# Performance work log

Hardware: AMD Instinct MI355X
Metric: run time of the kernel (lower is better)

Reference implementation:

```python
import jax, jax.numpy as jnp
import numpy as np

NW, NS, E = 50000, 10000, 100000
H, C = 6, 300            # heads, out_channels (word_size)
DIN_S, DIN_W = 640, 300  # sentence_size, word_size
DHID = 2048              # FFN hidden


def setup_inputs() -> dict:
    key = jax.random.key(0)
    ks = jax.random.split(key, 12)
    Hw = jax.random.normal(ks[0], (NW, DIN_W), dtype=jnp.float32)
    Hs = jax.random.normal(ks[1], (NS, DIN_S), dtype=jnp.float32)
    src = jax.random.randint(ks[2], (E,), 0, NS)
    dst = jax.random.randint(ks[3], (E,), 0, NW)
    s2w = jnp.stack([src, dst]).astype(jnp.int64)  # [2, E] edge_index
    # GATConv params (bipartite): lin_src, lin_dst, att_src, att_dst, bias
    Wsrc = jax.random.normal(ks[4], (H * C, DIN_S), dtype=jnp.float32) / np.sqrt(DIN_S)
    Wdst = jax.random.normal(ks[5], (H * C, DIN_W), dtype=jnp.float32) / np.sqrt(DIN_W)
    att_src = jax.random.normal(ks[6], (H, C), dtype=jnp.float32) / np.sqrt(C)
    att_dst = jax.random.normal(ks[7], (H, C), dtype=jnp.float32) / np.sqrt(C)
    bias_gat = jnp.zeros((H * C,), dtype=jnp.float32)
    # FFN params: Linear(1800 -> 2048), Linear(2048 -> 300)
    W1 = jax.random.normal(ks[8], (DHID, H * C), dtype=jnp.float32) / np.sqrt(H * C)
    b1 = jnp.zeros((DHID,), dtype=jnp.float32)
    W2 = jax.random.normal(ks[9], (DIN_W, DHID), dtype=jnp.float32) / np.sqrt(DHID)
    b2 = jnp.zeros((DIN_W,), dtype=jnp.float32)
    return dict(Hw=Hw, Hs=Hs, s2w=s2w, Wsrc=Wsrc, Wdst=Wdst, att_src=att_src,
                att_dst=att_dst, bias_gat=bias_gat, W1=W1, b1=b1, W2=W2, b2=b2)


def reference(Hw, Hs, s2w, Wsrc, Wdst, att_src, att_dst, bias_gat, W1, b1, W2, b2):
    nw = Hw.shape[0]
    src, dst = s2w[0], s2w[1]
    h, c = att_src.shape
    # edge-wise linear transforms (done node-wise, then gathered)
    xs = (Hs @ Wsrc.T).reshape(-1, h, c)   # [Ns, H, C]
    xd = (Hw @ Wdst.T).reshape(-1, h, c)   # [Nw, H, C]
    a_s = jnp.einsum('nhc,hc->nh', xs, att_src)  # [Ns, H]
    a_d = jnp.einsum('nhc,hc->nh', xd, att_dst)  # [Nw, H]
    alpha = a_s[src] + a_d[dst]                  # [E, H]
    alpha = jnp.where(alpha > 0, alpha, 0.2 * alpha)  # leaky_relu(0.2)
    # segment softmax over edges grouped by destination word
    m = jax.ops.segment_max(alpha, dst, num_segments=nw)      # [Nw, H]
    ex = jnp.exp(alpha - m[dst])                               # [E, H]
    den = jax.ops.segment_sum(ex, dst, num_segments=nw)       # [Nw, H]
    w = ex / den[dst]                                          # [E, H]
    msg = xs[src] * w[:, :, None]                              # [E, H, C]
    agg = jax.ops.segment_sum(msg, dst, num_segments=nw)      # [Nw, H, C]
    Uw = agg.reshape(nw, h * c) + bias_gat                     # concat heads + bias
    # activation (elu), dropout treated as identity (deterministic reference)
    Uw = jax.nn.elu(Uw)
    # FFN with residual to Hw
    out = (Uw @ W1.T + b1) @ W2.T + b2 + Hw
    return out
```

## Files before the change

### kernel.cpp

```cpp
#include <hip/hip_runtime.h>
#include <hip/hip_bf16.h>
#include <math.h>

#define NWn 50000
#define NSn 10000
#define NEn 100000
#define Hn  6
#define DWn 300
#define DSn 640
#define DHn 2048
#define HCn 1800
#define HCp 1824
#define K32 57
#define NFB 19
#define CHUNK 10000
#define ENC_NEGINF 0x007FFFFFu

typedef short bf16x8 __attribute__((ext_vector_type(8)));
typedef float f32x4  __attribute__((ext_vector_type(4)));

__device__ __forceinline__ unsigned enc_ord(float f) {
  unsigned u = __float_as_uint(f);
  return (u & 0x80000000u) ? ~u : (u | 0x80000000u);
}
__device__ __forceinline__ float dec_ord(unsigned u) {
  unsigned v = (u & 0x80000000u) ? (u ^ 0x80000000u) : ~u;
  return __uint_as_float(v);
}
__device__ __forceinline__ float eluf(float x) { return x > 0.0f ? x : expm1f(x); }
__device__ __forceinline__ float b2f(short s) {
  return __uint_as_float(((unsigned)(unsigned short)s) << 16);
}
__device__ __forceinline__ short f2b(float f) {
  __hip_bfloat16 h = __float2bfloat16(f);
  return *(short*)&h;
}

__device__ __forceinline__ int ld_src(const int* s32, int e, int f) {
  return f ? s32[2 * e] : s32[e];
}
__device__ __forceinline__ int ld_dst(const int* s32, int e, int f) {
  return f ? s32[2 * NEn + 2 * e] : s32[NEn + e];
}

__global__ __launch_bounds__(256) void k_init(unsigned* m_enc, float* den, int* deg,
                                              int* cur, int* flag, float* Vs, float* Vd) {
  int i = blockIdx.x * 256 + threadIdx.x;
  if (i < NWn * Hn) { m_enc[i] = ENC_NEGINF; den[i] = 0.0f; }
  if (i < NWn) { deg[i] = 0; cur[i] = 0; }
  if (i < Hn * DSn) Vs[i] = 0.f;
  if (i < Hn * DWn) Vd[i] = 0.f;
  if (i == 0) *flag = 1;
}

__global__ __launch_bounds__(256) void k_detect(const int* __restrict__ s32, int* flag) {
  int j = threadIdx.x;
  if (s32[2 * j + 1] != 0) atomicAnd(flag, 0);
}

__global__ __launch_bounds__(256) void k_cvt(const float* __restrict__ src,
    __hip_bfloat16* __restrict__ dst, int n4) {
  int i = blockIdx.x * 256 + threadIdx.x;
  if (i >= n4) return;
  float4 v = *(const float4*)&src[(size_t)i * 4];
  __hip_bfloat16 o[4] = {__float2bfloat16(v.x), __float2bfloat16(v.y),
                         __float2bfloat16(v.z), __float2bfloat16(v.w)};
  *(ulong1*)&dst[(size_t)i * 4] = *(ulong1*)o;
}

__global__ __launch_bounds__(256) void k_tcvt(const float* __restrict__ W1,
    __hip_bfloat16* __restrict__ W1t) {
  __shared__ __hip_bfloat16 T[64][65];
  int tid = threadIdx.x;
  int tx = tid & 15, ty = tid >> 4;
  int c0 = blockIdx.x * 64;
  int r0 = blockIdx.y * 64;
  #pragma unroll
  for (int rr = 0; rr < 4; ++rr) {
    int sr = r0 + rr * 16 + ty;
    int sc = c0 + tx * 4;
    float4 v;
    if (sc + 3 < HCn) {
      v = *(const float4*)&W1[(size_t)sr * HCn + sc];
    } else {
      v.x = (sc + 0 < HCn) ? W1[(size_t)sr * HCn + sc + 0] : 0.f;
      v.y = (sc + 1 < HCn) ? W1[(size_t)sr * HCn + sc + 1] : 0.f;
      v.z = (sc + 2 < HCn) ? W1[(size_t)sr * HCn + sc + 2] : 0.f;
      v.w = (sc + 3 < HCn) ? W1[(size_t)sr * HCn + sc + 3] : 0.f;
    }
    T[tx * 4 + 0][rr * 16 + ty] = __float2bfloat16(v.x);
    T[tx * 4 + 1][rr * 16 + ty] = __float2bfloat16(v.y);
    T[tx * 4 + 2][rr * 16 + ty] = __float2bfloat16(v.z);
    T[tx * 4 + 3][rr * 16 + ty] = __float2bfloat16(v.w);
  }
  __syncthreads();
  #pragma unroll
  for (int ww = 0; ww < 4; ++ww) {
    int dl = ww * 16 + ty;
    int dr = c0 + dl;
    if (dr >= HCn) continue;
    __hip_bfloat16 o[4] = {T[dl][tx * 4 + 0], T[dl][tx * 4 + 1],
                           T[dl][tx * 4 + 2], T[dl][tx * 4 + 3]};
    *(uint2*)&W1t[(size_t)dr * DHn + r0 + tx * 4] = *(uint2*)o;
  }
}

#define VCC 6
__global__ __launch_bounds__(256) void k_vsd(const float* __restrict__ Wsrc,
    const float* __restrict__ Wdst, const float* __restrict__ att_src,
    const float* __restrict__ att_dst, float* __restrict__ Vs, float* __restrict__ Vd) {
  int b = blockIdx.x;
  bool isD = b >= Hn * VCC;
  int bb = isD ? b - Hn * VCC : b;
  int h = bb / VCC, cc = bb % VCC;
  int cbeg = h * 300 + cc * 50, cend = cbeg + 50;
  if (!isD) {
    for (int k = threadIdx.x; k < DSn; k += 256) {
      float s = 0.f;
      for (int c = cbeg; c < cend; ++c)
        s = fmaf(att_src[c], Wsrc[(size_t)c * DSn + k], s);
      unsafeAtomicAdd(&Vs[h * DSn + k], s);
    }
  } else {
    for (int k = threadIdx.x; k < DWn; k += 256) {
      float s = 0.f;
      for (int c = cbeg; c < cend; ++c)
        s = fmaf(att_dst[c], Wdst[(size_t)c * DWn + k], s);
      unsafeAtomicAdd(&Vd[h * DWn + k], s);
    }
  }
}

__global__ __launch_bounds__(256) void k_rowdot(const float* __restrict__ X,
    const float* __restrict__ V, float* __restrict__ outv, int nrows, int K) {
  extern __shared__ float VL[];
  for (int i = threadIdx.x; i < Hn * K; i += 256) VL[i] = V[i];
  __syncthreads();
  int row = blockIdx.x * 4 + (threadIdx.x >> 6);
  int lane = threadIdx.x & 63;
  if (row >= nrows) return;
  float acc[Hn] = {0.f, 0.f, 0.f, 0.f, 0.f, 0.f};
  const float* xr = X + (size_t)row * K;
  for (int k = lane; k < K; k += 64) {
    float x = xr[k];
    #pragma unroll
    for (int h = 0; h < Hn; ++h) acc[h] = fmaf(x, VL[h * K + k], acc[h]);
  }
  #pragma unroll
  for (int h = 0; h < Hn; ++h) {
    float v = acc[h];
    for (int ofs = 32; ofs > 0; ofs >>= 1) v += __shfl_down(v, ofs);
    if (lane == 0) outv[(size_t)row * Hn + h] = v;
  }
}

__global__ __launch_bounds__(256) void k_bc(const float* __restrict__ W2,
    const float* __restrict__ b1, const float* __restrict__ b2, float* __restrict__ bc) {
  int j = blockIdx.x * 4 + (threadIdx.x >> 6);
  int lane = threadIdx.x & 63;
  if (j >= DWn) return;
  float s = 0.f;
  for (int t = lane; t < DHn; t += 64) s = fmaf(W2[(size_t)j * DHn + t], b1[t], s);
  for (int ofs = 32; ofs > 0; ofs >>= 1) s += __shfl_down(s, ofs);
  if (lane == 0) bc[j] = s + b2[j];
}

template <int EPI>
__global__ __launch_bounds__(256) void k_mfma(
    const __hip_bfloat16* __restrict__ A, const __hip_bfloat16* __restrict__ B,
    void* __restrict__ Cout, int M, int N, int K, int lda, int ldb, int ldc) {
  __shared__ short As[2][128 * 32];
  __shared__ short Bs[2][128 * 32];
  int tid = threadIdx.x, lane = tid & 63, wid = tid >> 6;
  int wr = wid >> 1, wc = wid & 1;
  int m0 = blockIdx.y * 128, n0 = blockIdx.x * 128;
  int z = blockIdx.z;
  int ksp = K / (int)gridDim.z;
  int kbeg = z * ksp;
  int nt = ksp / 32;
  auto STAGE = [&](int buf, int kk) {
    #pragma unroll
    for (int i = 0; i < 2; ++i) {
      int slotbase = wid * 128 + i * 64;
      int s = slotbase + lane;
      int row = s >> 2, kq = (s & 3) ^ ((row >> 1) & 3);
      int gm = m0 + row; if (gm > M - 1) gm = M - 1;
      const __hip_bfloat16* gsa = A + (size_t)gm * lda + kk + kq * 8;
      __builtin_amdgcn_global_load_lds(
          (const __attribute__((address_space(1))) void*)gsa,
          (__attribute__((address_space(3))) void*)&As[buf][slotbase * 8], 16, 0, 0);
      int gn = n0 + row; if (gn > N - 1) gn = N - 1;
      const __hip_bfloat16* gsb = B + (size_t)gn * ldb + kk + kq * 8;
      __builtin_amdgcn_global_load_lds(
          (const __attribute__((address_space(1))) void*)gsb,
          (__attribute__((address_space(3))) void*)&Bs[buf][slotbase * 8], 16, 0, 0);
    }
  };
  f32x4 acc[4][4] = {};
  STAGE(0, kbeg);
  int cur = 0;
  for (int t = 0; t < nt; ++t) {
    __builtin_amdgcn_s_barrier();
    if (t + 1 < nt) {
      STAGE(cur ^ 1, kbeg + (t + 1) * 32);
      asm volatile("s_waitcnt vmcnt(4)" ::: "memory");
    } else {
      asm volatile("s_waitcnt vmcnt(0)" ::: "memory");
    }
    __builtin_amdgcn_s_barrier();
    __builtin_amdgcn_sched_barrier(0);
    bf16x8 af[4], bfr[4];
    int kqw = lane >> 4;
    #pragma unroll
    for (int mf = 0; mf < 4; ++mf) {
      int ra = wr * 64 + mf * 16 + (lane & 15);
      af[mf] = *(bf16x8*)&As[cur][(ra * 4 + (kqw ^ ((ra >> 1) & 3))) * 8];
    }
    #pragma unroll
    for (int nf = 0; nf < 4; ++nf) {
      int rb = wc * 64 + nf * 16 + (lane & 15);
      bfr[nf] = *(bf16x8*)&Bs[cur][(rb * 4 + (kqw ^ ((rb >> 1) & 3))) * 8];
    }
    #pragma unroll
    for (int mf = 0; mf < 4; ++mf)
      #pragma unroll
      for (int nf = 0; nf < 4; ++nf)
        acc[mf][nf] = __builtin_amdgcn_mfma_f32_16x16x32_bf16(af[mf], bfr[nf],
                                                              acc[mf][nf], 0, 0, 0);
    cur ^= 1;
  }
  #pragma unroll
  for (int mf = 0; mf < 4; ++mf) {
    int gmb = m0 + wr * 64 + mf * 16 + (lane >> 4) * 4;
    #pragma unroll
    for (int nf = 0; nf < 4; ++nf) {
      int gn = n0 + wc * 64 + nf * 16 + (lane & 15);
      if (gn >= N) continue;
      #pragma unroll
      for (int r4 = 0; r4 < 4; ++r4) {
        int gm = gmb + r4;
        if (gm >= M) continue;
        if (EPI == 0)
          ((__hip_bfloat16*)Cout)[(size_t)gm * ldc + gn] = __float2bfloat16(acc[mf][nf][r4]);
        else
          ((float*)Cout)[((size_t)z * M + gm) * ldc + gn] = acc[mf][nf][r4];
      }
    }
  }
}

__global__ __launch_bounds__(256) void k_mfma_pa(
    const __hip_bfloat16* __restrict__ Apk, const __hip_bfloat16* __restrict__ Bpk,
    float* __restrict__ Cout, int M, int maxAf,
    const float* __restrict__ bc, const float* __restrict__ Hw, int rowbase) {
  int tid = threadIdx.x, lane = tid & 63, wid = tid >> 6;
  int wr = wid >> 1, wc = wid & 1;
  int nwg = (int)(gridDim.x * gridDim.y);
  int wg = (int)(blockIdx.y * gridDim.x + blockIdx.x);
  int q = nwg >> 3, r = nwg & 7;
  int xcd = wg & 7, idx = wg >> 3;
  int swz = (xcd < r) ? (xcd * (q + 1) + idx) : (r * (q + 1) + (xcd - r) * q + idx);
  int m0 = (swz / (int)gridDim.x) * 128, n0 = (swz % (int)gridDim.x) * 128;
  const short* Ab = (const short*)Apk;
  const short* Bb = (const short*)Bpk;
  int ra16[4], cb16[4];
  #pragma unroll
  for (int mf = 0; mf < 4; ++mf) {
    int v = (m0 >> 4) + wr * 4 + mf;
    ra16[mf] = v > maxAf ? maxAf : v;
  }
  #pragma unroll
  for (int nf = 0; nf < 4; ++nf) {
    int v = (n0 >> 4) + wc * 4 + nf;
    cb16[nf] = v > (NFB - 1) ? (NFB - 1) : v;
  }
  f32x4 acc[4][4] = {};
  for (int ks = 0; ks < K32; ++ks) {
    bf16x8 af[4], bfv[4];
    #pragma unroll
    for (int mf = 0; mf < 4; ++mf)
      af[mf] = *(const bf16x8*)&Ab[((size_t)ra16[mf] * K32 + ks) * 512 + lane * 8];
    #pragma unroll
    for (int nf = 0; nf < 4; ++nf)
      bfv[nf] = *(const bf16x8*)&Bb[((size_t)cb16[nf] * K32 + ks) * 512 + lane * 8];
    #pragma unroll
    for (int mf = 0; mf < 4; ++mf)
      #pragma unroll
      for (int nf = 0; nf < 4; ++nf)
        acc[mf][nf] = __builtin_amdgcn_mfma_f32_16x16x32_bf16(af[mf], bfv[nf],
                                                              acc[mf][nf], 0, 0, 0);
  }
  #pragma unroll
  for (int mf = 0; mf < 4; ++mf) {
    int gmb = m0 + wr * 64 + mf * 16 + (lane >> 4) * 4;
    #pragma unroll
    for (int nf = 0; nf < 4; ++nf) {
      int gn = n0 + wc * 64 + nf * 16 + (lane & 15);
      if (gn >= DWn) continue;
      #pragma unroll
      for (int r4 = 0; r4 < 4; ++r4) {
        int gm = gmb + r4;
        if (gm >= M) continue;
        size_t grow = (size_t)(rowbase + gm);
        Cout[grow * DWn + gn] = acc[mf][nf][r4] + bc[gn] + Hw[grow * DWn + gn];
      }
    }
  }
}

__global__ __launch_bounds__(256) void k_wc_reduce(const float* __restrict__ part,
    __hip_bfloat16* __restrict__ Bpk) {
  int i = blockIdx.x * 256 + threadIdx.x;
  if (i >= 16 * NFB * HCp) return;
  int m = i / HCp, n = i % HCp;
  float s = 0.f;
  if (m < DWn && n < HCn) {
    #pragma unroll
    for (int s8 = 0; s8 < 8; ++s8)
      s += part[((size_t)s8 * DWn + m) * HCp + n];
  }
  size_t frag = (size_t)(m >> 4) * K32 + (n >> 5);
  int lane = ((n >> 3) & 3) * 16 + (m & 15);
  Bpk[frag * 512 + lane * 8 + (n & 7)] = __float2bfloat16(s);
}

__global__ __launch_bounds__(256) void k_alpha(const int* __restrict__ s32,
    const int* __restrict__ flag, const float* __restrict__ a_s,
    const float* __restrict__ a_d, float* __restrict__ alpha,
    unsigned* __restrict__ m_enc, int* __restrict__ deg) {
  int e = blockIdx.x * 256 + threadIdx.x;
  if (e >= NEn) return;
  int f = *flag;
  int s = ld_src(s32, e, f), d = ld_dst(s32, e, f);
  atomicAdd(&deg[d], 1);
  #pragma unroll
  for (int h = 0; h < Hn; ++h) {
    float av = a_s[s * Hn + h] + a_d[d * Hn + h];
    float lr = av > 0.f ? av : 0.2f * av;
    alpha[(size_t)e * Hn + h] = lr;
    atomicMax(&m_enc[d * Hn + h], enc_ord(lr));
  }
}

__global__ __launch_bounds__(256) void k_ex(const int* __restrict__ s32,
    const int* __restrict__ flag, float* __restrict__ wgt,
    const unsigned* __restrict__ m_enc, float* __restrict__ den) {
  int e = blockIdx.x * 256 + threadIdx.x;
  if (e >= NEn) return;
  int d = ld_dst(s32, e, *flag);
  #pragma unroll
  for (int h = 0; h < Hn; ++h) {
    float mx = dec_ord(m_enc[d * Hn + h]);
    float exv = expf(wgt[(size_t)e * Hn + h] - mx);
    wgt[(size_t)e * Hn + h] = exv;
    unsafeAtomicAdd(&den[d * Hn + h], exv);
  }
}

__global__ __launch_bounds__(256) void k_scan1(const int* __restrict__ deg,
    int* __restrict__ off, int* __restrict__ bsum) {
  __shared__ int sh[256];
  int i = blockIdx.x * 256 + threadIdx.x;
  int v = (i < NWn) ? deg[i] : 0;
  sh[threadIdx.x] = v;
  __syncthreads();
  for (int ofs = 1; ofs < 256; ofs <<= 1) {
    int t = (threadIdx.x >= ofs) ? sh[threadIdx.x - ofs] : 0;
    __syncthreads();
    sh[threadIdx.x] += t;
    __syncthreads();
  }
  if (i < NWn) off[i] = sh[threadIdx.x] - v;
  if (threadIdx.x == 255) bsum[blockIdx.x] = sh[255];
}

__global__ __launch_bounds__(256) void k_scan2(const int* __restrict__ bsum,
    int* __restrict__ boff, int nb) {
  __shared__ int sh[256];
  int v = (threadIdx.x < nb) ? bsum[threadIdx.x] : 0;
  sh[threadIdx.x] = v;
  __syncthreads();
  for (int ofs = 1; ofs < 256; ofs <<= 1) {
    int t = (threadIdx.x >= ofs) ? sh[threadIdx.x - ofs] : 0;
    __syncthreads();
    sh[threadIdx.x] += t;
    __syncthreads();
  }
  if (threadIdx.x < nb) boff[threadIdx.x] = sh[threadIdx.x] - v;
}

__global__ __launch_bounds__(256) void k_scan3(int* __restrict__ off,
    const int* __restrict__ boff) {
  int i = blockIdx.x * 256 + threadIdx.x;
  if (i < NWn) off[i] += boff[blockIdx.x];
}

__global__ __launch_bounds__(256) void k_fill(const int* __restrict__ s32,
    const int* __restrict__ flag, const int* __restrict__ off,
    int* __restrict__ cur, int* __restrict__ eid) {
  int e = blockIdx.x * 256 + threadIdx.x;
  if (e >= NEn) return;
  int d = ld_dst(s32, e, *flag);
  int pos = off[d] + atomicAdd(&cur[d], 1);
  eid[pos] = e;
}

__global__ __launch_bounds__(256) void k_agg(const int* __restrict__ s32,
    const int* __restrict__ flag, const int* __restrict__ eid,
    const int* __restrict__ off, const __hip_bfloat16* __restrict__ xs,
    const float* __restrict__ wgt, const float* __restrict__ den,
    const float* __restrict__ bias_gat, __hip_bfloat16* __restrict__ aggP,
    int rowbase) {
  int rloc = blockIdx.x;
  int d = rowbase + rloc;
  int c0 = threadIdx.x * 8;
  if (c0 >= HCp) return;
  size_t frag = (size_t)(rloc >> 4) * K32 + (c0 >> 5);
  int plane = ((c0 >> 3) & 3) * 16 + (rloc & 15);
  short* dst = (short*)aggP + frag * 512 + plane * 8;
  if (c0 >= HCn) {
    bf16x8 zz = {};
    *(bf16x8*)dst = zz;
    return;
  }
  int f = *flag;
  int start = off[d];
  int end = (d == NWn - 1) ? NEn : off[d + 1];
  int hlo = c0 / 300, hhi = (c0 + 7) / 300;
  int split = (hlo == hhi) ? 8 : (hhi * 300 - c0);
  float acc[8] = {};
  for (int p = start; p < end; ++p) {
    int e = eid[p];
    int s = ld_src(s32, e, f);
    bf16x8 x = *(const bf16x8*)&xs[(size_t)s * HCn + c0];
    float wlo = wgt[(size_t)e * Hn + hlo];
    float whi = wgt[(size_t)e * Hn + hhi];
    #pragma unroll
    for (int j = 0; j < 8; ++j)
      acc[j] = fmaf((j < split) ? wlo : whi, b2f(x[j]), acc[j]);
  }
  float dlo = den[(size_t)d * Hn + hlo];
  float dhi = den[(size_t)d * Hn + hhi];
  float ilo = dlo > 0.f ? 1.0f / dlo : 0.f;
  float ihi = dhi > 0.f ? 1.0f / dhi : 0.f;
  float4 b0 = *(const float4*)&bias_gat[c0];
  float4 b1v = *(const float4*)&bias_gat[c0 + 4];
  float bb[8] = {b0.x, b0.y, b0.z, b0.w, b1v.x, b1v.y, b1v.z, b1v.w};
  bf16x8 o;
  #pragma unroll
  for (int j = 0; j < 8; ++j)
    o[j] = f2b(eluf(acc[j] * ((j < split) ? ilo : ihi) + bb[j]));
  *(bf16x8*)dst = o;
}

extern "C" void kernel_launch(void* const* d_in, const int* in_sizes, int n_in,
                              void* d_out, int out_size, void* d_ws, size_t ws_size,
                              hipStream_t stream) {
  const float* Hw       = (const float*)d_in[0];
  const float* Hs       = (const float*)d_in[1];
  const int*   s2w      = (const int*)d_in[2];
  const float* Wsrc     = (const float*)d_in[3];
  const float* Wdst     = (const float*)d_in[4];
  const float* att_src  = (const float*)d_in[5];
  const float* att_dst  = (const float*)d_in[6];
  const float* bias_gat = (const float*)d_in[7];
  const float* W1       = (const float*)d_in[8];
  const float* b1       = (const float*)d_in[9];
  const float* W2       = (const float*)d_in[10];
  const float* b2       = (const float*)d_in[11];
  float* out = (float*)d_out;

  char* ws = (char*)d_ws;
  size_t o = 0;
  auto alloc = [&](size_t bytes) {
    size_t cur = o;
    o = (o + bytes + 255) & ~(size_t)255;
    return cur;
  };
  __hip_bfloat16* xs    = (__hip_bfloat16*)(ws + alloc(2ull * NSn * HCn));
  __hip_bfloat16* Wsrcb = (__hip_bfloat16*)(ws + alloc(2ull * HCn * DSn));
  __hip_bfloat16* Bpk   = (__hip_bfloat16*)(ws + alloc(2ull * NFB * K32 * 512));
  float*    bc    = (float*)(ws + alloc(sizeof(float) * DWn));
  float*    Vs    = (float*)(ws + alloc(sizeof(float) * Hn * DSn));
  float*    Vd    = (float*)(ws + alloc(sizeof(float) * Hn * DWn));
  float*    a_s   = (float*)(ws + alloc(sizeof(float) * (size_t)NSn * Hn));
  float*    a_d   = (float*)(ws + alloc(sizeof(float) * (size_t)NWn * Hn));
  float*    wgt   = (float*)(ws + alloc(sizeof(float) * (size_t)NEn * Hn));
  unsigned* m_enc = (unsigned*)(ws + alloc(sizeof(unsigned) * (size_t)NWn * Hn));
  float*    den   = (float*)(ws + alloc(sizeof(float) * (size_t)NWn * Hn));
  int*      deg   = (int*)(ws + alloc(sizeof(int) * NWn));
  int*      offr  = (int*)(ws + alloc(sizeof(int) * NWn));
  int*      cur   = (int*)(ws + alloc(sizeof(int) * NWn));
  int*      eid   = (int*)(ws + alloc(sizeof(int) * NEn));
  int*      bsum  = (int*)(ws + alloc(sizeof(int) * 256));
  int*      boff  = (int*)(ws + alloc(sizeof(int) * 256));
  int*      flag  = (int*)(ws + alloc(sizeof(int) * 64));
  size_t region = o;
  size_t ro = region;
  auto ralloc = [&](size_t bytes) {
    size_t cur2 = ro;
    ro = (ro + bytes + 255) & ~(size_t)255;
    return cur2;
  };
  __hip_bfloat16* Hsb = (__hip_bfloat16*)(ws + ralloc(2ull * NSn * DSn));
  __hip_bfloat16* W2b = (__hip_bfloat16*)(ws + ralloc(2ull * DWn * DHn));
  __hip_bfloat16* W1t = (__hip_bfloat16*)(ws + ralloc(2ull * HCn * DHn));
  float*          WcP = (float*)(ws + ralloc(4ull * 8 * DWn * HCp));
  size_t region_small_end = ro;
  size_t big_end = region + 2ull * NWn * HCp;
  bool bigpath = (big_end <= ws_size);
  __hip_bfloat16* aggc;
  if (bigpath) {
    aggc = (__hip_bfloat16*)(ws + region);
  } else {
    o = region_small_end;
    aggc = (__hip_bfloat16*)(ws + alloc(2ull * CHUNK * HCp));
    if (o > ws_size) return;
  }
  (void)in_sizes; (void)n_in; (void)out_size;

  const int NWB = (NWn + 255) / 256;

  k_init<<<dim3((NWn * Hn + 255) / 256), dim3(256), 0, stream>>>(
      m_enc, den, deg, cur, flag, Vs, Vd);
  k_detect<<<dim3(1), dim3(256), 0, stream>>>(s2w, flag);
  k_cvt<<<dim3((NSn * DSn / 4 + 255) / 256), dim3(256), 0, stream>>>(Hs, Hsb, NSn * DSn / 4);
  k_cvt<<<dim3((HCn * DSn / 4 + 255) / 256), dim3(256), 0, stream>>>(Wsrc, Wsrcb, HCn * DSn / 4);
  k_cvt<<<dim3((DWn * DHn / 4 + 255) / 256), dim3(256), 0, stream>>>(W2, W2b, DWn * DHn / 4);
  k_tcvt<<<dim3((HCn + 63) / 64, DHn / 64), dim3(256), 0, stream>>>(W1, W1t);
  k_vsd<<<dim3(2 * Hn * VCC), dim3(256), 0, stream>>>(
      Wsrc, Wdst, att_src, att_dst, Vs, Vd);
  k_bc<<<dim3((DWn + 3) / 4), dim3(256), 0, stream>>>(W2, b1, b2, bc);
  k_mfma<2><<<dim3((HCn + 127) / 128, (DWn + 127) / 128, 8), dim3(256), 0, stream>>>(
      W2b, W1t, WcP, DWn, HCn, DHn, DHn, DHn, HCp);
  k_wc_reduce<<<dim3((16 * NFB * HCp + 255) / 256), dim3(256), 0, stream>>>(WcP, Bpk);
  k_rowdot<<<dim3((NSn + 3) / 4), dim3(256), Hn * DSn * sizeof(float), stream>>>(
      Hs, Vs, a_s, NSn, DSn);
  k_rowdot<<<dim3((NWn + 3) / 4), dim3(256), Hn * DWn * sizeof(float), stream>>>(
      Hw, Vd, a_d, NWn, DWn);
  k_mfma<0><<<dim3((HCn + 127) / 128, (NSn + 127) / 128, 1), dim3(256), 0, stream>>>(
      Hsb, Wsrcb, xs, NSn, HCn, DSn, DSn, DSn, HCn);
  k_alpha<<<dim3((NEn + 255) / 256), dim3(256), 0, stream>>>(
      s2w, flag, a_s, a_d, wgt, m_enc, deg);
  k_ex<<<dim3((NEn + 255) / 256), dim3(256), 0, stream>>>(s2w, flag, wgt, m_enc, den);
  k_scan1<<<dim3(NWB), dim3(256), 0, stream>>>(deg, offr, bsum);
  k_scan2<<<dim3(1), dim3(256), 0, stream>>>(bsum, boff, NWB);
  k_scan3<<<dim3(NWB), dim3(256), 0, stream>>>(offr, boff);
  k_fill<<<dim3((NEn + 255) / 256), dim3(256), 0, stream>>>(s2w, flag, offr, cur, eid);
  if (bigpath) {
    k_agg<<<dim3(NWn), dim3(256), 0, stream>>>(
        s2w, flag, eid, offr, xs, wgt, den, bias_gat, aggc, 0);
    k_mfma_pa<<<dim3(3, (NWn + 127) / 128), dim3(256), 0, stream>>>(
        aggc, Bpk, out, NWn, NWn / 16 - 1, bc, Hw, 0);
  } else {
    for (int c = 0; c < NWn / CHUNK; ++c) {
      int rowbase = c * CHUNK;
      k_agg<<<dim3(CHUNK), dim3(256), 0, stream>>>(
          s2w, flag, eid, offr, xs, wgt, den, bias_gat, aggc, rowbase);
      k_mfma_pa<<<dim3(3, (CHUNK + 127) / 128), dim3(256), 0, stream>>>(
          aggc, Bpk, out, CHUNK, CHUNK / 16 - 1, bc, Hw, rowbase);
    }
  }
}
```

Measured before the change: 654.5 us.

## Aggregate 16 rows per block via LDS staging; prefetch next K-step in MFMA GEMM

k_agg now handles 16 destination rows per block, sequentially accumulates each row's edges into a shared-memory tile, then writes the MFMA-packed fragment layout with fully contiguous stores instead of scattered 16-byte writes. k_mfma_pa gains register double-buffering that loads the next K-slice fragments before issuing the current MFMAs, plus a launch-bounds occupancy hint. The aggregation launches 16x fewer blocks, each doing serial per-row loops, which may reduce parallelism and latency hiding for the gather. The extra prefetch registers may also pressure occupancy.

Result: slower. 709.7 us (+8.4%).

```diff
diff --git a/kernel.cpp b/kernel.cpp
--- a/kernel.cpp
+++ b/kernel.cpp
@@ -14,6 +14,7 @@
 #define K32 57
 #define NFB 19
 #define CHUNK 10000
+#define AGPAD 1832
 #define ENC_NEGINF 0x007FFFFFu
 
 typedef short bf16x8 __attribute__((ext_vector_type(8)));
@@ -249,7 +250,7 @@
   }
 }
 
-__global__ __launch_bounds__(256) void k_mfma_pa(
+__global__ __launch_bounds__(256, 3) void k_mfma_pa(
     const __hip_bfloat16* __restrict__ Apk, const __hip_bfloat16* __restrict__ Bpk,
     float* __restrict__ Cout, int M, int maxAf,
     const float* __restrict__ bc, const float* __restrict__ Hw, int rowbase) {
@@ -275,20 +276,34 @@
     cb16[nf] = v > (NFB - 1) ? (NFB - 1) : v;
   }
   f32x4 acc[4][4] = {};
+  bf16x8 cA[4], cB[4], nA[4], nB[4];
+  #pragma unroll
+  for (int mf = 0; mf < 4; ++mf)
+    cA[mf] = *(const bf16x8*)&Ab[(size_t)ra16[mf] * K32 * 512 + lane * 8];
+  #pragma unroll
+  for (int nf = 0; nf < 4; ++nf)
+    cB[nf] = *(const bf16x8*)&Bb[(size_t)cb16[nf] * K32 * 512 + lane * 8];
   for (int ks = 0; ks < K32; ++ks) {
-    bf16x8 af[4], bfv[4];
+    if (ks + 1 < K32) {
+      #pragma unroll
+      for (int mf = 0; mf < 4; ++mf)
+        nA[mf] = *(const bf16x8*)&Ab[((size_t)ra16[mf] * K32 + ks + 1) * 512 + lane * 8];
+      #pragma unroll
+      for (int nf = 0; nf < 4; ++nf)
+        nB[nf] = *(const bf16x8*)&Bb[((size_t)cb16[nf] * K32 + ks + 1) * 512 + lane * 8];
+    }
     #pragma unroll
     for (int mf = 0; mf < 4; ++mf)
-      af[mf] = *(const bf16x8*)&Ab[((size_t)ra16[mf] * K32 + ks) * 512 + lane * 8];
-    #pragma unroll
-    for (int nf = 0; nf < 4; ++nf)
-      bfv[nf] = *(const bf16x8*)&Bb[((size_t)cb16[nf] * K32 + ks) * 512 + lane * 8];
-    #pragma unroll
-    for (int mf = 0; mf < 4; ++mf)
       #pragma unroll
       for (int nf = 0; nf < 4; ++nf)
-        acc[mf][nf] = __builtin_amdgcn_mfma_f32_16x16x32_bf16(af[mf], bfv[nf],
+        acc[mf][nf] = __builtin_amdgcn_mfma_f32_16x16x32_bf16(cA[mf], cB[nf],
                                                               acc[mf][nf], 0, 0, 0);
+    if (ks + 1 < K32) {
+      #pragma unroll
+      for (int mf = 0; mf < 4; ++mf) cA[mf] = nA[mf];
+      #pragma unroll
+      for (int nf = 0; nf < 4; ++nf) cB[nf] = nB[nf];
+    }
   }
   #pragma unroll
   for (int mf = 0; mf < 4; ++mf) {
@@ -411,46 +426,56 @@
     const float* __restrict__ wgt, const float* __restrict__ den,
     const float* __restrict__ bias_gat, __hip_bfloat16* __restrict__ aggP,
     int rowbase) {
-  int rloc = blockIdx.x;
-  int d = rowbase + rloc;
-  int c0 = threadIdx.x * 8;
-  if (c0 >= HCp) return;
-  size_t frag = (size_t)(rloc >> 4) * K32 + (c0 >> 5);
-  int plane = ((c0 >> 3) & 3) * 16 + (rloc & 15);
-  short* dst = (short*)aggP + frag * 512 + plane * 8;
-  if (c0 >= HCn) {
-    bf16x8 zz = {};
-    *(bf16x8*)dst = zz;
-    return;
-  }
+  __shared__ short L[16][AGPAD];
+  int g = blockIdx.x;
+  int t = threadIdx.x;
+  int c0 = t * 8;
   int f = *flag;
-  int start = off[d];
-  int end = (d == NWn - 1) ? NEn : off[d + 1];
-  int hlo = c0 / 300, hhi = (c0 + 7) / 300;
-  int split = (hlo == hhi) ? 8 : (hhi * 300 - c0);
-  float acc[8] = {};
-  for (int p = start; p < end; ++p) {
-    int e = eid[p];
-    int s = ld_src(s32, e, f);
-    bf16x8 x = *(const bf16x8*)&xs[(size_t)s * HCn + c0];
-    float wlo = wgt[(size_t)e * Hn + hlo];
-    float whi = wgt[(size_t)e * Hn + hhi];
-    #pragma unroll
-    for (int j = 0; j < 8; ++j)
-      acc[j] = fmaf((j < split) ? wlo : whi, b2f(x[j]), acc[j]);
-  }
-  float dlo = den[(size_t)d * Hn + hlo];
-  float dhi = den[(size_t)d * Hn + hhi];
-  float ilo = dlo > 0.f ? 1.0f / dlo : 0.f;
-  float ihi = dhi > 0.f ? 1.0f / dhi : 0.f;
-  float4 b0 = *(const float4*)&bias_gat[c0];
-  float4 b1v = *(const float4*)&bias_gat[c0 + 4];
-  float bb[8] = {b0.x, b0.y, b0.z, b0.w, b1v.x, b1v.y, b1v.z, b1v.w};
-  bf16x8 o;
-  #pragma unroll
-  for (int j = 0; j < 8; ++j)
-    o[j] = f2b(eluf(acc[j] * ((j < split) ? ilo : ihi) + bb[j]));
-  *(bf16x8*)dst = o;
+  if (c0 < HCp) {
+    if (c0 >= HCn) {
+      bf16x8 zz = {};
+      #pragma unroll
+      for (int r = 0; r < 16; ++r) *(bf16x8*)&L[r][c0] = zz;
+    } else {
+      int hlo = c0 / 300, hhi = (c0 + 7) / 300;
+      int split = (hlo == hhi) ? 8 : (hhi * 300 - c0);
+      float4 b0 = *(const float4*)&bias_gat[c0];
+      float4 b1v = *(const float4*)&bias_gat[c0 + 4];
+      float bb[8] = {b0.x, b0.y, b0.z, b0.w, b1v.x, b1v.y, b1v.z, b1v.w};
+      for (int r = 0; r < 16; ++r) {
+        int d = rowbase + g * 16 + r;
+        float acc[8] = {};
+        int start = off[d];
+        int end = (d == NWn - 1) ? NEn : off[d + 1];
+        for (int p = start; p < end; ++p) {
+          int e = eid[p];
+          int s = ld_src(s32, e, f);
+          bf16x8 x = *(const bf16x8*)&xs[(size_t)s * HCn + c0];
+          float wlo = wgt[(size_t)e * Hn + hlo];
+          float whi = wgt[(size_t)e * Hn + hhi];
+          #pragma unroll
+          for (int j = 0; j < 8; ++j)
+            acc[j] = fmaf((j < split) ? wlo : whi, b2f(x[j]), acc[j]);
+        }
+        float dlo = den[(size_t)d * Hn + hlo];
+        float dhi = den[(size_t)d * Hn + hhi];
+        float ilo = dlo > 0.f ? 1.0f / dlo : 0.f;
+        float ihi = dhi > 0.f ? 1.0f / dhi : 0.f;
+        bf16x8 o;
+        #pragma unroll
+        for (int j = 0; j < 8; ++j)
+          o[j] = f2b(eluf(acc[j] * ((j < split) ? ilo : ihi) + bb[j]));
+        *(bf16x8*)&L[r][c0] = o;
+      }
+    }
+  }
+  __syncthreads();
+  short* base = (short*)aggP + (size_t)g * K32 * 512;
+  for (int w = t; w < K32 * 64; w += 256) {
+    int ks = w >> 6, lane = w & 63;
+    bf16x8 v = *(const bf16x8*)&L[lane & 15][ks * 32 + (lane >> 4) * 8];
+    *(bf16x8*)&base[(size_t)w * 8] = v;
+  }
 }
 
 extern "C" void kernel_launch(void* const* d_in, const int* in_sizes, int n_in,
@@ -548,14 +573,14 @@
   k_scan3<<<dim3(NWB), dim3(256), 0, stream>>>(offr, boff);
   k_fill<<<dim3((NEn + 255) / 256), dim3(256), 0, stream>>>(s2w, flag, offr, cur, eid);
   if (bigpath) {
-    k_agg<<<dim3(NWn), dim3(256), 0, stream>>>(
+    k_agg<<<dim3(NWn / 16), dim3(256), 0, stream>>>(
         s2w, flag, eid, offr, xs, wgt, den, bias_gat, aggc, 0);
     k_mfma_pa<<<dim3(3, (NWn + 127) / 128), dim3(256), 0, stream>>>(
         aggc, Bpk, out, NWn, NWn / 16 - 1, bc, Hw, 0);
   } else {
     for (int c = 0; c < NWn / CHUNK; ++c) {
       int rowbase = c * CHUNK;
-      k_agg<<<dim3(CHUNK), dim3(256), 0, stream>>>(
+      k_agg<<<dim3(CHUNK / 16), dim3(256), 0, stream>>>(
           s2w, flag, eid, offr, xs, wgt, den, bias_gat, aggc, rowbase);
       k_mfma_pa<<<dim3(3, (CHUNK + 127) / 128), dim3(256), 0, stream>>>(
           aggc, Bpk, out, CHUNK, CHUNK / 16 - 1, bc, Hw, rowbase);
```

## Switch final GEMM operands to row-major layout with register prefetch

Applied to the files above, without the earlier changes.

Replaces the fragment-packed layouts of the aggregated activations and the combined FFN weight with plain row-major buffers of padded width. The final MFMA kernel now loads each k-slice directly from row-major rows, software-pipelines the next slice into registers while the current MFMAs run, and requests three waves per SIMD in its launch bounds. This simplifies the k_agg and k_wc_reduce stores, but the per-lane loads in the GEMM become strided 16-byte reads from different rows instead of one contiguous 1 KB fragment per wave, and the double-buffered registers raise register pressure.

After: 654.3 us. No clear change (-0.0%).

```diff
diff --git a/kernel.cpp b/kernel.cpp
--- a/kernel.cpp
+++ b/kernel.cpp
@@ -12,7 +12,7 @@
 #define HCn 1800
 #define HCp 1824
 #define K32 57
-#define NFB 19
+#define NBP 304
 #define CHUNK 10000
 #define ENC_NEGINF 0x007FFFFFu
 
@@ -249,9 +249,9 @@
   }
 }
 
-__global__ __launch_bounds__(256) void k_mfma_pa(
-    const __hip_bfloat16* __restrict__ Apk, const __hip_bfloat16* __restrict__ Bpk,
-    float* __restrict__ Cout, int M, int maxAf,
+__global__ __launch_bounds__(256, 3) void k_mfma_pa(
+    const __hip_bfloat16* __restrict__ Agg, const __hip_bfloat16* __restrict__ Wcb,
+    float* __restrict__ Cout, int M,
     const float* __restrict__ bc, const float* __restrict__ Hw, int rowbase) {
   int tid = threadIdx.x, lane = tid & 63, wid = tid >> 6;
   int wr = wid >> 1, wc = wid & 1;
@@ -261,34 +261,52 @@
   int xcd = wg & 7, idx = wg >> 3;
   int swz = (xcd < r) ? (xcd * (q + 1) + idx) : (r * (q + 1) + (xcd - r) * q + idx);
   int m0 = (swz / (int)gridDim.x) * 128, n0 = (swz % (int)gridDim.x) * 128;
-  const short* Ab = (const short*)Apk;
-  const short* Bb = (const short*)Bpk;
-  int ra16[4], cb16[4];
+  const short* Ab = (const short*)Agg;
+  const short* Bb = (const short*)Wcb;
+  size_t arow[4], brow[4];
   #pragma unroll
   for (int mf = 0; mf < 4; ++mf) {
-    int v = (m0 >> 4) + wr * 4 + mf;
-    ra16[mf] = v > maxAf ? maxAf : v;
+    int gm = m0 + wr * 64 + mf * 16 + (lane & 15);
+    if (gm > M - 1) gm = M - 1;
+    arow[mf] = (size_t)gm * HCp;
   }
   #pragma unroll
   for (int nf = 0; nf < 4; ++nf) {
-    int v = (n0 >> 4) + wc * 4 + nf;
-    cb16[nf] = v > (NFB - 1) ? (NFB - 1) : v;
-  }
+    int gn = n0 + wc * 64 + nf * 16 + (lane & 15);
+    if (gn > NBP - 1) gn = NBP - 1;
+    brow[nf] = (size_t)gn * HCp;
+  }
+  int klane = (lane >> 4) * 8;
   f32x4 acc[4][4] = {};
+  bf16x8 cA[4], cB[4], nA[4], nB[4];
+  #pragma unroll
+  for (int mf = 0; mf < 4; ++mf)
+    cA[mf] = *(const bf16x8*)&Ab[arow[mf] + klane];
+  #pragma unroll
+  for (int nf = 0; nf < 4; ++nf)
+    cB[nf] = *(const bf16x8*)&Bb[brow[nf] + klane];
   for (int ks = 0; ks < K32; ++ks) {
-    bf16x8 af[4], bfv[4];
+    if (ks + 1 < K32) {
+      int kn = (ks + 1) * 32 + klane;
+      #pragma unroll
+      for (int mf = 0; mf < 4; ++mf)
+        nA[mf] = *(const bf16x8*)&Ab[arow[mf] + kn];
+      #pragma unroll
+      for (int nf = 0; nf < 4; ++nf)
+        nB[nf] = *(const bf16x8*)&Bb[brow[nf] + kn];
+    }
     #pragma unroll
     for (int mf = 0; mf < 4; ++mf)
-      af[mf] = *(const bf16x8*)&Ab[((size_t)ra16[mf] * K32 + ks) * 512 + lane * 8];
-    #pragma unroll
-    for (int nf = 0; nf < 4; ++nf)
-      bfv[nf] = *(const bf16x8*)&Bb[((size_t)cb16[nf] * K32 + ks) * 512 + lane * 8];
-    #pragma unroll
-    for (int mf = 0; mf < 4; ++mf)
       #pragma unroll
       for (int nf = 0; nf < 4; ++nf)
-        acc[mf][nf] = __builtin_amdgcn_mfma_f32_16x16x32_bf16(af[mf], bfv[nf],
+        acc[mf][nf] = __builtin_amdgcn_mfma_f32_16x16x32_bf16(cA[mf], cB[nf],
                                                               acc[mf][nf], 0, 0, 0);
+    if (ks + 1 < K32) {
+      #pragma unroll
+      for (int mf = 0; mf < 4; ++mf) cA[mf] = nA[mf];
+      #pragma unroll
+      for (int nf = 0; nf < 4; ++nf) cB[nf] = nB[nf];
+    }
   }
   #pragma unroll
   for (int mf = 0; mf < 4; ++mf) {
@@ -309,9 +327,9 @@
 }
 
 __global__ __launch_bounds__(256) void k_wc_reduce(const float* __restrict__ part,
-    __hip_bfloat16* __restrict__ Bpk) {
+    __hip_bfloat16* __restrict__ Wcb) {
   int i = blockIdx.x * 256 + threadIdx.x;
-  if (i >= 16 * NFB * HCp) return;
+  if (i >= NBP * HCp) return;
   int m = i / HCp, n = i % HCp;
   float s = 0.f;
   if (m < DWn && n < HCn) {
@@ -319,9 +337,7 @@
     for (int s8 = 0; s8 < 8; ++s8)
       s += part[((size_t)s8 * DWn + m) * HCp + n];
   }
-  size_t frag = (size_t)(m >> 4) * K32 + (n >> 5);
-  int lane = ((n >> 3) & 3) * 16 + (m & 15);
-  Bpk[frag * 512 + lane * 8 + (n & 7)] = __float2bfloat16(s);
+  Wcb[i] = __float2bfloat16(s);
 }
 
 __global__ __launch_bounds__(256) void k_alpha(const int* __restrict__ s32,
@@ -409,18 +425,14 @@
     const int* __restrict__ flag, const int* __restrict__ eid,
     const int* __restrict__ off, const __hip_bfloat16* __restrict__ xs,
     const float* __restrict__ wgt, const float* __restrict__ den,
-    const float* __restrict__ bias_gat, __hip_bfloat16* __restrict__ aggP,
+    const float* __restrict__ bias_gat, __hip_bfloat16* __restrict__ aggc,
     int rowbase) {
-  int rloc = blockIdx.x;
-  int d = rowbase + rloc;
+  int d = rowbase + blockIdx.x;
   int c0 = threadIdx.x * 8;
   if (c0 >= HCp) return;
-  size_t frag = (size_t)(rloc >> 4) * K32 + (c0 >> 5);
-  int plane = ((c0 >> 3) & 3) * 16 + (rloc & 15);
-  short* dst = (short*)aggP + frag * 512 + plane * 8;
   if (c0 >= HCn) {
     bf16x8 zz = {};
-    *(bf16x8*)dst = zz;
+    *(bf16x8*)&aggc[(size_t)blockIdx.x * HCp + c0] = zz;
     return;
   }
   int f = *flag;
@@ -450,7 +462,7 @@
   #pragma unroll
   for (int j = 0; j < 8; ++j)
     o[j] = f2b(eluf(acc[j] * ((j < split) ? ilo : ihi) + bb[j]));
-  *(bf16x8*)dst = o;
+  *(bf16x8*)&aggc[(size_t)blockIdx.x * HCp + c0] = o;
 }
 
 extern "C" void kernel_launch(void* const* d_in, const int* in_sizes, int n_in,
@@ -479,7 +491,7 @@
   };
   __hip_bfloat16* xs    = (__hip_bfloat16*)(ws + alloc(2ull * NSn * HCn));
   __hip_bfloat16* Wsrcb = (__hip_bfloat16*)(ws + alloc(2ull * HCn * DSn));
-  __hip_bfloat16* Bpk   = (__hip_bfloat16*)(ws + alloc(2ull * NFB * K32 * 512));
+  __hip_bfloat16* Wcb   = (__hip_bfloat16*)(ws + alloc(2ull * NBP * HCp));
   float*    bc    = (float*)(ws + alloc(sizeof(float) * DWn));
   float*    Vs    = (float*)(ws + alloc(sizeof(float) * Hn * DSn));
   float*    Vd    = (float*)(ws + alloc(sizeof(float) * Hn * DWn));
@@ -533,7 +545,7 @@
   k_bc<<<dim3((DWn + 3) / 4), dim3(256), 0, stream>>>(W2, b1, b2, bc);
   k_mfma<2><<<dim3((HCn + 127) / 128, (DWn + 127) / 128, 8), dim3(256), 0, stream>>>(
       W2b, W1t, WcP, DWn, HCn, DHn, DHn, DHn, HCp);
-  k_wc_reduce<<<dim3((16 * NFB * HCp + 255) / 256), dim3(256), 0, stream>>>(WcP, Bpk);
+  k_wc_reduce<<<dim3((NBP * HCp + 255) / 256), dim3(256), 0, stream>>>(WcP, Wcb);
   k_rowdot<<<dim3((NSn + 3) / 4), dim3(256), Hn * DSn * sizeof(float), stream>>>(
       Hs, Vs, a_s, NSn, DSn);
   k_rowdot<<<dim3((NWn + 3) / 4), dim3(256), Hn * DWn * sizeof(float), stream>>>(
@@ -551,14 +563,14 @@
     k_agg<<<dim3(NWn), dim3(256), 0, stream>>>(
         s2w, flag, eid, offr, xs, wgt, den, bias_gat, aggc, 0);
     k_mfma_pa<<<dim3(3, (NWn + 127) / 128), dim3(256), 0, stream>>>(
-        aggc, Bpk, out, NWn, NWn / 16 - 1, bc, Hw, 0);
+        aggc, Wcb, out, NWn, bc, Hw, 0);
   } else {
     for (int c = 0; c < NWn / CHUNK; ++c) {
       int rowbase = c * CHUNK;
       k_agg<<<dim3(CHUNK), dim3(256), 0, stream>>>(
           s2w, flag, eid, offr, xs, wgt, den, bias_gat, aggc, rowbase);
       k_mfma_pa<<<dim3(3, (CHUNK + 127) / 128), dim3(256), 0, stream>>>(
-          aggc, Bpk, out, CHUNK, CHUNK / 16 - 1, bc, Hw, rowbase);
-    }
-  }
-}
+          aggc, Wcb, out, CHUNK, bc, Hw, rowbase);
+    }
+  }
+}
```
